# Kernel optimization log

Hardware: AMD Instinct MI355X
Metric: run time of the kernel (lower is better)

## Reference

```python
import jax, jax.numpy as jnp
import numpy as np

EPS = 1e-5
K = 20


def knn_idx(x, k):
    # x: (B, C, N) -> idx: (B, N, k) of nearest neighbors (self included)
    sq = jnp.sum(x * x, axis=1)  # (B, N)
    # pd[b,n,m] = -||x_n - x_m||^2
    pd = 2.0 * jnp.einsum('bcn,bcm->bnm', x, x) - sq[:, :, None] - sq[:, None, :]
    return jax.lax.top_k(pd, k)[1]


def graph_feature(x, k):
    # x: (B, C, N) -> (B, N, k, 2C) = concat(center, neighbor - center)
    idx = knn_idx(x, k)
    xt = jnp.transpose(x, (0, 2, 1))  # (B, N, C)
    nbr = jax.vmap(lambda t, i: t[i])(xt, idx)  # (B, N, k, C)
    ctr = jnp.broadcast_to(xt[:, :, None, :], nbr.shape)
    return jnp.concatenate([ctr, nbr - ctr], axis=-1)


def conv_bn_lrelu2d(feat, w, g, b):
    # 1x1 Conv2d (bias=False) + BatchNorm2d (training stats) + LeakyReLU(0.2)
    y = jnp.einsum('bnkc,oc->bonk', feat, w)  # (B, O, N, k)
    m = jnp.mean(y, axis=(0, 2, 3), keepdims=True)
    v = jnp.var(y, axis=(0, 2, 3), keepdims=True)
    y = (y - m) / jnp.sqrt(v + EPS) * g[None, :, None, None] + b[None, :, None, None]
    return jax.nn.leaky_relu(y, 0.2)


def reference(x, w1, g1, b1, w2, g2, b2, w3, g3, b3, w4, g4, b4, w5, g5, b5):
    x1 = jnp.max(conv_bn_lrelu2d(graph_feature(x, K), w1, g1, b1), axis=-1)   # (B, 64, N)
    x2 = jnp.max(conv_bn_lrelu2d(graph_feature(x1, K), w2, g2, b2), axis=-1)  # (B, 64, N)
    x3 = jnp.max(conv_bn_lrelu2d(graph_feature(x2, K), w3, g3, b3), axis=-1)  # (B, 128, N)
    x4 = jnp.max(conv_bn_lrelu2d(graph_feature(x3, K), w4, g4, b4), axis=-1)  # (B, 256, N)
    xc = jnp.concatenate([x1, x2, x3, x4], axis=1)  # (B, 512, N)
    y = jnp.einsum('bcn,oc->bon', xc, w5)  # (B, 1024, N)
    m = jnp.mean(y, axis=(0, 2), keepdims=True)
    v = jnp.var(y, axis=(0, 2), keepdims=True)
    y = (y - m) / jnp.sqrt(v + EPS) * g5[None, :, None] + b5[None, :, None]
    y = jax.nn.leaky_relu(y, 0.2)
    return jnp.max(y, axis=-1)  # (B, 1024)


def setup_inputs() -> dict:
    key = jax.random.key(0)
    ks = jax.random.split(key, 6)
    B, N = 8, 2048
    s = 0.02
    return {
        'x': jax.random.normal(ks[0], (B, 3, N), dtype=jnp.float32),
        'w1': jax.random.normal(ks[1], (64, 6), dtype=jnp.float32) * s,
        'g1': jnp.ones((64,), jnp.float32), 'b1': jnp.zeros((64,), jnp.float32),
        'w2': jax.random.normal(ks[2], (64, 128), dtype=jnp.float32) * s,
        'g2': jnp.ones((64,), jnp.float32), 'b2': jnp.zeros((64,), jnp.float32),
        'w3': jax.random.normal(ks[3], (128, 128), dtype=jnp.float32) * s,
        'g3': jnp.ones((128,), jnp.float32), 'b3': jnp.zeros((128,), jnp.float32),
        'w4': jax.random.normal(ks[4], (256, 256), dtype=jnp.float32) * s,
        'g4': jnp.ones((256,), jnp.float32), 'b4': jnp.zeros((256,), jnp.float32),
        'w5': jax.random.normal(ks[5], (1024, 512), dtype=jnp.float32) * s,
        'g5': jnp.ones((1024,), jnp.float32), 'b5': jnp.zeros((1024,), jnp.float32),
    }
```

## Files before the change

### kernel.cpp

```cpp
#include <hip/hip_runtime.h>
#include <hip/hip_bf16.h>
#include <math.h>

#define BB 8
#define NN 2048
#define KK 20
#define XCCH 512
#define NSLOT 64
#define LEPS 1e-5f
#define NEGINF -3.4e38f

typedef __attribute__((ext_vector_type(8))) short s8v;
typedef __attribute__((ext_vector_type(8))) _Float16 h8v;
typedef __attribute__((ext_vector_type(4))) float f32x4;

__device__ __forceinline__ float lrelu(float x){ return x >= 0.f ? x : 0.2f*x; }

__global__ __launch_bounds__(256) void k_transpose(const float* __restrict__ x, float* __restrict__ xt){
  int i = blockIdx.x*256 + threadIdx.x;
  if (i >= BB*NN) return;
  int b = i >> 11, n = i & (NN-1);
  float4 v;
  v.x = x[(b*3+0)*NN + n];
  v.y = x[(b*3+1)*NN + n];
  v.z = x[(b*3+2)*NN + n];
  v.w = 0.f;
  reinterpret_cast<float4*>(xt)[i] = v;
}

__global__ __launch_bounds__(256) void k_cvtw(const float* __restrict__ W, __hip_bfloat16* __restrict__ Wb,
                                              int Cs, int coff, int Ccnt, int Cpad, int total){
  int i = blockIdx.x*256 + threadIdx.x;
  if (i >= total) return;
  int o = i / Cpad, c = i - o*Cpad;
  Wb[i] = (c < Ccnt) ? __float2bfloat16(W[(size_t)o*Cs + coff + c]) : __float2bfloat16(0.f);
}

__global__ __launch_bounds__(256) void k_split(const float* __restrict__ P, int stride, int Ci, int Cpad,
    _Float16* __restrict__ Ph, _Float16* __restrict__ Pl){
  int i = blockIdx.x*256 + threadIdx.x;
  if (i >= BB*NN*Cpad) return;
  int p = i / Cpad, c = i - p*Cpad;
  float v = (c < Ci) ? P[(size_t)p*stride + c] : 0.f;
  _Float16 h = (_Float16)v;
  float r = v - (float)h;
  Ph[i] = h;
  Pl[i] = (_Float16)r;
}

__global__ __launch_bounds__(256) void k_sqs(const _Float16* __restrict__ Ph,
    const _Float16* __restrict__ Pl, int Cpad, float* __restrict__ sq){
  int i = blockIdx.x*256 + threadIdx.x;
  if (i >= BB*NN) return;
  const _Float16* ph = Ph + (size_t)i*Cpad;
  const _Float16* pl = Pl + (size_t)i*Cpad;
  float s = 0.f;
  for (int c = 0; c < Cpad; ++c){
    float v = (float)ph[c] + (float)pl[c];
    s += v*v;
  }
  sq[i] = s;
}

__global__ __launch_bounds__(256) void k_distm(
    const _Float16* __restrict__ Ph, const _Float16* __restrict__ Pl,
    int Cpad, int nchunk, const float* __restrict__ sq, float* __restrict__ pd)
{
  __shared__ _Float16 Ah[128*40];
  __shared__ _Float16 Al[128*40];
  __shared__ _Float16 Bh[128*40];
  __shared__ _Float16 Bl[128*40];
  int t = threadIdx.x;
  int w = t >> 6, lane = t & 63, m = lane & 15, quad = lane >> 4;
  int b = blockIdx.z;
  int i = blockIdx.x;
  int by = (int)((sqrtf(8.f*(float)i + 1.f) - 1.f) * 0.5f);
  while ((by+1)*(by+2)/2 <= i) by++;
  while (by*(by+1)/2 > i) by--;
  int bx = i - by*(by+1)/2;
  int n0 = by * 128, m0 = bx * 128;
  const _Float16* PhB = Ph + (size_t)b*NN*Cpad;
  const _Float16* PlB = Pl + (size_t)b*NN*Cpad;
  f32x4 acc[2][8];
  #pragma unroll
  for (int s=0;s<2;s++)
    #pragma unroll
    for (int j=0;j<8;j++){ f32x4 z = {0.f,0.f,0.f,0.f}; acc[s][j] = z; }
  int r = t >> 1;
  int sg0 = t & 1;
  for (int ch=0; ch<nchunk; ++ch){
    int c0 = ch*32;
    #pragma unroll
    for (int k=0;k<2;k++){
      int seg = sg0 + 2*k;
      int go = c0 + seg*8;
      size_t an = (size_t)(n0+r)*Cpad + go;
      size_t bm = (size_t)(m0+r)*Cpad + go;
      *(h8v*)&Ah[r*40 + seg*8] = *(const h8v*)&PhB[an];
      *(h8v*)&Al[r*40 + seg*8] = *(const h8v*)&PlB[an];
      *(h8v*)&Bh[r*40 + seg*8] = *(const h8v*)&PhB[bm];
      *(h8v*)&Bl[r*40 + seg*8] = *(const h8v*)&PlB[bm];
    }
    __syncthreads();
    h8v ah0 = *(const h8v*)&Ah[(w*32 + m)*40 + quad*8];
    h8v al0 = *(const h8v*)&Al[(w*32 + m)*40 + quad*8];
    h8v ah1 = *(const h8v*)&Ah[(w*32 + 16 + m)*40 + quad*8];
    h8v al1 = *(const h8v*)&Al[(w*32 + 16 + m)*40 + quad*8];
    #pragma unroll
    for (int j=0;j<8;j++){
      h8v bh = *(const h8v*)&Bh[(j*16 + m)*40 + quad*8];
      h8v bl = *(const h8v*)&Bl[(j*16 + m)*40 + quad*8];
      acc[0][j] = __builtin_amdgcn_mfma_f32_16x16x32_f16(ah0, bh, acc[0][j], 0, 0, 0);
      acc[0][j] = __builtin_amdgcn_mfma_f32_16x16x32_f16(ah0, bl, acc[0][j], 0, 0, 0);
      acc[0][j] = __builtin_amdgcn_mfma_f32_16x16x32_f16(al0, bh, acc[0][j], 0, 0, 0);
      acc[0][j] = __builtin_amdgcn_mfma_f32_16x16x32_f16(al0, bl, acc[0][j], 0, 0, 0);
      acc[1][j] = __builtin_amdgcn_mfma_f32_16x16x32_f16(ah1, bh, acc[1][j], 0, 0, 0);
      acc[1][j] = __builtin_amdgcn_mfma_f32_16x16x32_f16(ah1, bl, acc[1][j], 0, 0, 0);
      acc[1][j] = __builtin_amdgcn_mfma_f32_16x16x32_f16(al1, bh, acc[1][j], 0, 0, 0);
      acc[1][j] = __builtin_amdgcn_mfma_f32_16x16x32_f16(al1, bl, acc[1][j], 0, 0, 0);
    }
    __syncthreads();
  }
  float sqm_[8];
  #pragma unroll
  for (int j=0;j<8;j++) sqm_[j] = sq[b*NN + m0 + j*16 + m];
  float sqn_[2][4];
  #pragma unroll
  for (int s=0;s<2;s++)
    #pragma unroll
    for (int rg=0; rg<4; rg++)
      sqn_[s][rg] = sq[b*NN + n0 + w*32 + s*16 + quad*4 + rg];
  #pragma unroll
  for (int s=0;s<2;s++){
    #pragma unroll
    for (int rg=0; rg<4; rg++){
      size_t rowoff = ((size_t)b*NN + n0 + w*32 + s*16 + quad*4 + rg)*NN + m0 + m;
      #pragma unroll
      for (int j=0;j<8;j++){
        pd[rowoff + j*16] = 2.f*acc[s][j][rg] - sqn_[s][rg] - sqm_[j];
      }
    }
  }
  if (bx != by){
    #pragma unroll
    for (int s=0;s<2;s++){
      #pragma unroll
      for (int j=0;j<8;j++){
        size_t moff = ((size_t)b*NN + m0 + j*16 + m)*NN + n0 + w*32 + s*16 + quad*4;
        float4 v;
        v.x = 2.f*acc[s][j][0] - sqm_[j] - sqn_[s][0];
        v.y = 2.f*acc[s][j][1] - sqm_[j] - sqn_[s][1];
        v.z = 2.f*acc[s][j][2] - sqm_[j] - sqn_[s][2];
        v.w = 2.f*acc[s][j][3] - sqm_[j] - sqn_[s][3];
        *(float4*)&pd[moff] = v;
      }
    }
  }
}

#define TK_REP32(F) F(0)F(1)F(2)F(3)F(4)F(5)F(6)F(7)F(8)F(9)F(10)F(11)F(12)F(13)F(14)F(15) \
                    F(16)F(17)F(18)F(19)F(20)F(21)F(22)F(23)F(24)F(25)F(26)F(27)F(28)F(29)F(30)F(31)
#define TK3_SCAN(u) { bool c1 = r##u > p1; bool c2 = r##u > p2; bool c3 = r##u > p3; \
    p3 = c2 ? p2 : (c3 ? r##u : p3); \
    i2 = c1 ? i1 : (c2 ? u : i2); \
    p2 = c1 ? p1 : (c2 ? r##u : p2); \
    i1 = c1 ? u : i1; \
    p1 = c1 ? r##u : p1; }
#define TK3_RSCAN(u) { float vv = ((rem >> u) & 1u) ? NEGINF : r##u; \
    bool c1 = vv > p1; bool c2 = vv > p2; bool c3 = vv > p3; \
    p3 = c2 ? p2 : (c3 ? vv : p3); \
    i2 = c1 ? i1 : (c2 ? u : i2); \
    p2 = c1 ? p1 : (c2 ? vv : p2); \
    i1 = c1 ? u : i1; \
    p1 = c1 ? vv : p1; }

__global__ __launch_bounds__(256) void k_topk(const float* __restrict__ pd, int* __restrict__ idxo){
  int t = threadIdx.x;
  int l = t & 63;
  int row = blockIdx.x*4 + (t >> 6);
  const float4* rp = (const float4*)(pd + (size_t)row*NN);
  float4 q0 = rp[0*64+l], q1 = rp[1*64+l], q2 = rp[2*64+l], q3 = rp[3*64+l];
  float4 q4 = rp[4*64+l], q5 = rp[5*64+l], q6 = rp[6*64+l], q7 = rp[7*64+l];
  float r0 =q0.x, r1 =q0.y, r2 =q0.z, r3 =q0.w, r4 =q1.x, r5 =q1.y, r6 =q1.z, r7 =q1.w;
  float r8 =q2.x, r9 =q2.y, r10=q2.z, r11=q2.w, r12=q3.x, r13=q3.y, r14=q3.z, r15=q3.w;
  float r16=q4.x, r17=q4.y, r18=q4.z, r19=q4.w, r20=q5.x, r21=q5.y, r22=q5.z, r23=q5.w;
  float r24=q6.x, r25=q6.y, r26=q6.z, r27=q6.w, r28=q7.x, r29=q7.y, r30=q7.z, r31=q7.w;
  float p1 = NEGINF, p2 = NEGINF, p3 = NEGINF;
  int i1 = 0, i2 = 0, nv = 3;
  unsigned rem = 0u;
  TK_REP32(TK3_SCAN)
  int* orow = idxo + (size_t)row*KK;
  int got = 0;
  while (got < KK){
    float M2 = p2;
    #pragma unroll
    for (int off=1; off<64; off<<=1) M2 = fmaxf(M2, __shfl_xor(M2, off));
    bool ex = (p1 >= M2);
    unsigned long long ball = __ballot(ex);
    int cnt = __popcll(ball);
    int take = KK - got;
    if (cnt <= take){
      if (ex){
        int pos = got + __popcll(ball & ((1ull << l) - 1ull));
        orow[pos] = ((i1 >> 2) << 8) | (l << 2) | (i1 & 3);
        rem |= 1u << i1;
        p1 = p2; i1 = i2; p2 = p3; nv--;
      }
      got += cnt;
      if (got < KK && nv < 2){
        p1 = NEGINF; p2 = NEGINF; p3 = NEGINF; i1 = 0; i2 = 0;
        TK_REP32(TK3_RSCAN)
        nv = 3;
      }
    } else {
      for (int tt = 0; tt < take; ++tt){
        float wv = p1;
        #pragma unroll
        for (int off=1; off<64; off<<=1) wv = fmaxf(wv, __shfl_xor(wv, off));
        int gi = (p1 == wv) ? (((i1 >> 2) << 8) | (l << 2) | (i1 & 3)) : 0x7FFFFFFF;
        int cand = gi;
        #pragma unroll
        for (int off=1; off<64; off<<=1){
          int oc = __shfl_xor(cand, off);
          cand = oc < cand ? oc : cand;
        }
        if (gi == cand){
          orow[got + tt] = cand;
          p1 = NEGINF;
        }
      }
      got = KK;
    }
  }
}

__global__ __launch_bounds__(256) void k_wprep(const float* __restrict__ W, int Ci, int Oi,
                                               float* __restrict__ W2){
  int i = blockIdx.x*256 + threadIdx.x;
  if (i >= 2*Oi*Ci) return;
  int r = i / Ci, c = i - r*Ci;
  if (r < Oi){
    W2[i] = W[(size_t)r*2*Ci + Ci + c];
  } else {
    int o = r - Oi;
    W2[i] = W[(size_t)o*2*Ci + c] - W[(size_t)o*2*Ci + Ci + c];
  }
}

__global__ __launch_bounds__(256) void k_gemmud(const float* __restrict__ P, int stride, int Ci,
    const float* __restrict__ W2, int ostr, float* __restrict__ udb){
  __shared__ float Pt[16*68];
  __shared__ float Wt[16*68];
  int t = threadIdx.x, ty = t >> 4, tx = t & 15;
  int p0 = blockIdx.x*64, o0 = blockIdx.y*64;
  float acc[4][4];
  #pragma unroll
  for (int i=0;i<4;i++)
    #pragma unroll
    for (int j=0;j<4;j++) acc[i][j]=0.f;
  for (int c0 = 0; c0 < Ci; c0 += 16){
    #pragma unroll
    for (int q=0;q<4;q++){
      int e = t + 256*q;
      int r = e >> 4, cc = e & 15;
      int c = c0 + cc;
      bool ok = (c < Ci);
      Pt[cc*68 + r] = ok ? P[(size_t)(p0+r)*stride + c] : 0.f;
      Wt[cc*68 + r] = ok ? W2[(size_t)(o0+r)*Ci + c] : 0.f;
    }
    __syncthreads();
    #pragma unroll
    for (int j=0;j<16;j++){
      float4 av  = *(const float4*)&Pt[j*68 + ty*4];
      float4 bv4 = *(const float4*)&Wt[j*68 + tx*4];
      float a[4]  = {av.x, av.y, av.z, av.w};
      float bv[4] = {bv4.x, bv4.y, bv4.z, bv4.w};
      #pragma unroll
      for (int i=0;i<4;i++)
        #pragma unroll
        for (int jj=0;jj<4;jj++) acc[i][jj] += a[i]*bv[jj];
    }
    __syncthreads();
  }
  #pragma unroll
  for (int i=0;i<4;i++){
    *(float4*)&udb[(size_t)(p0+ty*4+i)*ostr + o0 + tx*4] =
      make_float4(acc[i][0], acc[i][1], acc[i][2], acc[i][3]);
  }
}

__global__ __launch_bounds__(256) void k_edge(const float* __restrict__ udb, int ostr, int Oi,
    const int* __restrict__ idxg,
    float* __restrict__ ymax, float* __restrict__ ymin,
    float* __restrict__ chsum, float* __restrict__ chsq){
  __shared__ int lidx[16*KK];
  __shared__ float reds[2][4][64];
  int t = threadIdx.x, w = t >> 6, lane = t & 63;
  int n0 = blockIdx.x*16;
  int b  = n0 >> 11;
  int o0 = blockIdx.y*64;
  for (int q=t; q<16*KK; q+=256) lidx[q] = idxg[(size_t)n0*KK + q];
  __syncthreads();
  int o = o0 + lane;
  float ws_s = 0.f, ws_q = 0.f;
  #pragma unroll
  for (int p=0;p<4;p++){
    int pl = w*4 + p;
    int n = n0 + pl;
    float mx = -3.4e38f, mn = 3.4e38f, s = 0.f, s2 = 0.f;
    #pragma unroll
    for (int k=0;k<KK;k++){
      int nb = lidx[pl*KK + k];
      float u = udb[(size_t)((b<<11) + nb)*ostr + o];
      mx = fmaxf(mx, u); mn = fminf(mn, u);
      s += u; s2 += u*u;
    }
    float Dv = udb[(size_t)n*ostr + Oi + o];
    size_t base = (size_t)n*256 + o;
    ymax[base] = mx + Dv;
    ymin[base] = mn + Dv;
    ws_s += s + (float)KK*Dv;
    ws_q += s2 + 2.f*Dv*s + (float)KK*Dv*Dv;
  }
  reds[0][w][lane] = ws_s;
  reds[1][w][lane] = ws_q;
  __syncthreads();
  if (w == 0){
    float s = reds[0][0][lane] + reds[0][1][lane] + reds[0][2][lane] + reds[0][3][lane];
    float q = reds[1][0][lane] + reds[1][1][lane] + reds[1][2][lane] + reds[1][3][lane];
    int slot = blockIdx.x & (NSLOT-1);
    atomicAdd(&chsum[slot*256 + o], s);
    atomicAdd(&chsq [slot*256 + o], q);
  }
}

__global__ __launch_bounds__(256) void k_bnstats(const float* __restrict__ chsum, const float* __restrict__ chsq,
    const float* __restrict__ g, const float* __restrict__ bet,
    float* __restrict__ scl, float* __restrict__ shf, int Oi){
  int o = threadIdx.x;
  if (o >= Oi) return;
  float s=0.f, s2=0.f;
  for (int u=0;u<NSLOT;u++){ s += chsum[u*256+o]; s2 += chsq[u*256+o]; }
  float cnt = (float)(BB*NN*KK);
  float mean = s/cnt;
  float var = s2/cnt - mean*mean;
  float sc = g[o] / sqrtf(var + LEPS);
  scl[o] = sc;
  shf[o] = bet[o] - mean*sc;
}

__global__ __launch_bounds__(256) void k_apply(const float* __restrict__ ymax, const float* __restrict__ ymin,
    const float* __restrict__ scl, const float* __restrict__ shf,
    float* __restrict__ xc, __hip_bfloat16* __restrict__ xcb, int off, int Oi){
  int i = blockIdx.x*256 + threadIdx.x;
  if (i >= BB*NN*Oi) return;
  int o = i & (Oi-1);
  size_t p = (size_t)((unsigned)i / (unsigned)Oi);
  float sc = scl[o];
  float v = (sc >= 0.f) ? ymax[p*256+o] : ymin[p*256+o];
  float r = lrelu(v*sc + shf[o]);
  xc [p*XCCH + off + o] = r;
  xcb[p*XCCH + off + o] = __float2bfloat16(r);
}

__global__ __launch_bounds__(256) void k_conv5m(const __hip_bfloat16* __restrict__ xcb,
    const __hip_bfloat16* __restrict__ w5b,
    float* __restrict__ pmax, float* __restrict__ pmin,
    float* __restrict__ psum, float* __restrict__ psq)
{
  __shared__ __align__(16) char smem[20480];
  __hip_bfloat16* As = (__hip_bfloat16*)smem;
  __hip_bfloat16* Bs = (__hip_bfloat16*)(smem + 10240);
  float* red = (float*)smem;
  int t = threadIdx.x, w = t >> 6, lane = t & 63, m = lane & 15, quad = lane >> 4;
  int nbk = blockIdx.x;
  int b = blockIdx.z;
  int o0 = blockIdx.y * 128;
  int n0 = nbk * 128;
  const __hip_bfloat16* Abase = xcb + (size_t)(b*NN + n0)*XCCH;
  const __hip_bfloat16* Bbase = w5b + (size_t)o0*XCCH;
  f32x4 acc[2][8];
  #pragma unroll
  for (int s=0;s<2;s++)
    #pragma unroll
    for (int j=0;j<8;j++){ f32x4 z = {0.f,0.f,0.f,0.f}; acc[s][j] = z; }
  int r = t >> 1;
  int sg0 = t & 1;
  for (int ch=0; ch<16; ++ch){
    int c0 = ch*32;
    #pragma unroll
    for (int k=0;k<2;k++){
      int seg = sg0 + 2*k;
      int go = c0 + seg*8;
      *(s8v*)&As[r*40 + seg*8] = *(const s8v*)&Abase[(size_t)r*XCCH + go];
      *(s8v*)&Bs[r*40 + seg*8] = *(const s8v*)&Bbase[(size_t)r*XCCH + go];
    }
    __syncthreads();
    s8v a0 = *(const s8v*)&As[(w*32 + m)*40 + quad*8];
    s8v a1 = *(const s8v*)&As[(w*32 + 16 + m)*40 + quad*8];
    #pragma unroll
    for (int j=0;j<8;j++){
      s8v bf = *(const s8v*)&Bs[(j*16 + m)*40 + quad*8];
      acc[0][j] = __builtin_amdgcn_mfma_f32_16x16x32_bf16(a0, bf, acc[0][j], 0, 0, 0);
      acc[1][j] = __builtin_amdgcn_mfma_f32_16x16x32_bf16(a1, bf, acc[1][j], 0, 0, 0);
    }
    __syncthreads();
  }
  float mx[8], mn[8], sm[8], sq[8];
  #pragma unroll
  for (int j=0;j<8;j++){
    mx[j] = -3.4e38f; mn[j] = 3.4e38f; sm[j] = 0.f; sq[j] = 0.f;
    #pragma unroll
    for (int s=0;s<2;s++){
      f32x4 a = acc[s][j];
      #pragma unroll
      for (int rg=0; rg<4; rg++){
        float v = a[rg];
        mx[j] = fmaxf(mx[j], v); mn[j] = fminf(mn[j], v);
        sm[j] += v; sq[j] += v*v;
      }
    }
  }
  #pragma unroll
  for (int j=0;j<8;j++){
    #pragma unroll
    for (int off=16; off<=32; off<<=1){
      mx[j] = fmaxf(mx[j], __shfl_xor(mx[j], off));
      mn[j] = fminf(mn[j], __shfl_xor(mn[j], off));
      sm[j] += __shfl_xor(sm[j], off);
      sq[j] += __shfl_xor(sq[j], off);
    }
  }
  if (quad == 0){
    #pragma unroll
    for (int j=0;j<8;j++){
      int c = j*16 + m;
      red[(0*4 + w)*128 + c] = mx[j];
      red[(1*4 + w)*128 + c] = mn[j];
      red[(2*4 + w)*128 + c] = sm[j];
      red[(3*4 + w)*128 + c] = sq[j];
    }
  }
  __syncthreads();
  if (t < 128){
    int c = t;
    float MX = red[(0*4+0)*128+c], MN = red[(1*4+0)*128+c];
    float S  = red[(2*4+0)*128+c], Q  = red[(3*4+0)*128+c];
    #pragma unroll
    for (int u=1;u<4;u++){
      MX = fmaxf(MX, red[(0*4+u)*128+c]);
      MN = fminf(MN, red[(1*4+u)*128+c]);
      S += red[(2*4+u)*128+c];
      Q += red[(3*4+u)*128+c];
    }
    size_t ii = ((size_t)b*1024 + o0 + c)*16 + nbk;
    pmax[ii] = MX; pmin[ii] = MN; psum[ii] = S; psq[ii] = Q;
  }
}

__global__ __launch_bounds__(256) void k_stats5(const float* __restrict__ psum, const float* __restrict__ psq,
    const float* __restrict__ g5, const float* __restrict__ b5,
    float* __restrict__ sc5, float* __restrict__ sh5){
  int o = blockIdx.x*256 + threadIdx.x;
  float s=0.f, s2=0.f;
  for (int b=0;b<BB;b++){
    const float* ps = &psum[((size_t)b*1024 + o)*16];
    const float* pq = &psq [((size_t)b*1024 + o)*16];
    #pragma unroll
    for (int u=0;u<16;u++){ s += ps[u]; s2 += pq[u]; }
  }
  float cnt = (float)(BB*NN);
  float mean = s/cnt;
  float var = s2/cnt - mean*mean;
  float sc = g5[o] / sqrtf(var + LEPS);
  sc5[o] = sc;
  sh5[o] = b5[o] - mean*sc;
}

__global__ __launch_bounds__(256) void k_apply5(const float* __restrict__ pmax, const float* __restrict__ pmin,
    const float* __restrict__ sc5, const float* __restrict__ sh5, float* __restrict__ out){
  int i = blockIdx.x*256 + threadIdx.x;
  int o = i & 1023;
  float sc = sc5[o];
  float v;
  if (sc >= 0.f){
    const float* p = &pmax[(size_t)i*16];
    v = p[0];
    #pragma unroll
    for (int u=1;u<16;u++) v = fmaxf(v, p[u]);
  } else {
    const float* p = &pmin[(size_t)i*16];
    v = p[0];
    #pragma unroll
    for (int u=1;u<16;u++) v = fminf(v, p[u]);
  }
  out[i] = lrelu(v*sc + sh5[o]);
}

extern "C" void kernel_launch(void* const* d_in, const int* in_sizes, int n_in,
                              void* d_out, int out_size, void* d_ws, size_t ws_size,
                              hipStream_t stream){
  const float* x  = (const float*)d_in[0];
  const float* w1 = (const float*)d_in[1];
  const float* g1 = (const float*)d_in[2];
  const float* b1 = (const float*)d_in[3];
  const float* w2 = (const float*)d_in[4];
  const float* g2 = (const float*)d_in[5];
  const float* b2 = (const float*)d_in[6];
  const float* w3 = (const float*)d_in[7];
  const float* g3 = (const float*)d_in[8];
  const float* b3 = (const float*)d_in[9];
  const float* w4 = (const float*)d_in[10];
  const float* g4 = (const float*)d_in[11];
  const float* b4 = (const float*)d_in[12];
  const float* w5 = (const float*)d_in[13];
  const float* g5 = (const float*)d_in[14];
  const float* b5 = (const float*)d_in[15];
  float* out = (float*)d_out;
  float* ws = (float*)d_ws;

  const size_t F_PD   = 0;
  const size_t F_XT0  = F_PD   + (size_t)BB*NN*NN;
  const size_t F_XC   = F_XT0  + (size_t)BB*NN*4;
  const size_t F_CHS  = F_XC   + (size_t)BB*NN*XCCH;
  const size_t F_CHQ  = F_CHS  + (size_t)NSLOT*256;
  const size_t F_SCL  = F_CHQ  + (size_t)NSLOT*256;
  const size_t F_SHF  = F_SCL  + 256;
  const size_t F_SQ   = F_SHF  + 256;
  const size_t F_IDX  = F_SQ   + (size_t)BB*NN;
  const size_t F_PMAX = F_IDX  + (size_t)BB*NN*KK;
  const size_t F_PMIN = F_PMAX + (size_t)BB*1024*8;
  const size_t F_PSUM = F_PMIN + (size_t)BB*1024*8;
  const size_t F_PSQ  = F_PSUM + (size_t)BB*1024*8;
  const size_t F_SC5  = F_PSQ  + (size_t)BB*1024*8;
  const size_t F_SH5  = F_SC5  + 1024;
  const size_t F_XCB  = F_SH5  + 1024;
  const size_t F_WB   = F_XCB  + (size_t)BB*NN*XCCH/2;
  const size_t F_PH   = F_WB   + 278528;
  const size_t F_PL   = F_PH   + 1048576;

  float* pd    = ws + F_PD;
  float* udb   = pd;
  float* w2buf = pd + (size_t)12*1024*1024;
  float* ymax  = pd + (size_t)16*1024*1024;
  float* ymin  = pd + (size_t)21*1024*1024;
  float* pmax  = pd;
  float* pmin  = pd + (size_t)(1<<20);
  float* psum  = pd + (size_t)(2<<20);
  float* psq   = pd + (size_t)(3<<20);
  float* xt0   = ws + F_XT0;
  float* xc    = ws + F_XC;
  float* chsum = ws + F_CHS;
  float* chsq  = ws + F_CHQ;
  float* scl   = ws + F_SCL;
  float* shf   = ws + F_SHF;
  float* sqb   = ws + F_SQ;
  int*   idxb  = (int*)(ws + F_IDX);
  float* sc5   = ws + F_SC5;
  float* sh5   = ws + F_SH5;
  __hip_bfloat16* xcb = (__hip_bfloat16*)(ws + F_XCB);
  __hip_bfloat16* wb  = (__hip_bfloat16*)(ws + F_WB);
  __hip_bfloat16* w5b = wb + 32768;
  _Float16* Ph  = (_Float16*)(ws + F_PH);
  _Float16* Pl  = (_Float16*)(ws + F_PL);

  (void)in_sizes; (void)n_in; (void)out_size; (void)ws_size;

  k_transpose<<<64, 256, 0, stream>>>(x, xt0);
  k_cvtw<<<(524288+255)/256, 256, 0, stream>>>(w5, w5b, 512, 0, 512, 512, 524288);

  struct LayerP { const float* P; int stride; int Ci; int CiD; int Cpad;
                  const float* W; const float* g; const float* b; int Oi; int off; };
  LayerP L[4] = {
    { xt0,    4,   3,   4,   32,  w1, g1, b1,  64, 0   },
    { xc,     512, 64,  64,  64,  w2, g2, b2,  64, 64  },
    { xc+64,  512, 64,  64,  64,  w3, g3, b3, 128, 128 },
    { xc+128, 512, 128, 128, 128, w4, g4, b4, 256, 256 },
  };

  for (int l=0; l<4; ++l){
    int Cpad = L[l].Cpad, nchunk = Cpad/32;
    int Oi = L[l].Oi, Ci = L[l].Ci;
    int ostr = 2*Oi;
    k_split<<<(BB*NN*Cpad+255)/256, 256, 0, stream>>>(L[l].P, L[l].stride, L[l].CiD, Cpad, Ph, Pl);
    k_sqs<<<64, 256, 0, stream>>>(Ph, Pl, Cpad, sqb);
    k_distm<<<dim3(136,1,8), 256, 0, stream>>>(Ph, Pl, Cpad, nchunk, sqb, pd);
    k_topk<<<BB*NN/4, 256, 0, stream>>>(pd, idxb);
    hipMemsetAsync(chsum, 0, (size_t)NSLOT*256*2*sizeof(float), stream);
    k_wprep<<<(2*Oi*Ci+255)/256, 256, 0, stream>>>(L[l].W, Ci, Oi, w2buf);
    k_gemmud<<<dim3(BB*NN/64, ostr/64), 256, 0, stream>>>(L[l].P, L[l].stride, Ci, w2buf, ostr, udb);
    k_edge<<<dim3(BB*NN/16, Oi/64), 256, 0, stream>>>(udb, ostr, Oi, idxb, ymax, ymin, chsum, chsq);
    k_bnstats<<<1, 256, 0, stream>>>(chsum, chsq, L[l].g, L[l].b, scl, shf, Oi);
    k_apply<<<(BB*NN*Oi + 255)/256, 256, 0, stream>>>(ymax, ymin, scl, shf, xc, xcb, L[l].off, Oi);
  }

  k_conv5m<<<dim3(16, 8, BB), 256, 0, stream>>>(xcb, w5b, pmax, pmin, psum, psq);
  k_stats5<<<4, 256, 0, stream>>>(psum, psq, g5, b5, sc5, sh5);
  k_apply5<<<(BB*1024)/256, 256, 0, stream>>>(pmax, pmin, sc5, sh5, out);
}
```

Before: 676.4 us.

## Use split-fp16 MFMA GEMM for layer 4 and fuse fp16 split into apply

Layer 4's pointwise GEMM (Ci=128, 512 outputs) moves from a scalar fp32 FMA kernel to an MFMA kernel that uses hi/lo fp16 splits of activations and weights, with four products per tile to keep near-fp32 accuracy. The apply kernel now also writes the hi/lo fp16 split of its output for the next layer, which removes the separate split kernel for layers 2-4. It also skips the fp32 xc write for layers whose outputs are only read through the fp16 split. The cost is four MFMAs per tile plus extra fp16 stores in apply, and the result depends on the split-fp16 precision holding.

After: 646.4 us. -4.4%, faster.

```diff
diff --git a/kernel.cpp b/kernel.cpp
--- a/kernel.cpp
+++ b/kernel.cpp
@@ -289,6 +289,88 @@
   }
 }
 
+__global__ __launch_bounds__(256) void k_wprep2(const float* __restrict__ W, int Ci, int Cpad, int Oi,
+                                                _Float16* __restrict__ W2h, _Float16* __restrict__ W2l){
+  int i = blockIdx.x*256 + threadIdx.x;
+  if (i >= 2*Oi*Cpad) return;
+  int rr = i / Cpad, c = i - rr*Cpad;
+  float v = 0.f;
+  if (c < Ci){
+    if (rr < Oi) v = W[(size_t)rr*2*Ci + Ci + c];
+    else { int o = rr - Oi; v = W[(size_t)o*2*Ci + c] - W[(size_t)o*2*Ci + Ci + c]; }
+  }
+  _Float16 h = (_Float16)v;
+  W2h[i] = h;
+  W2l[i] = (_Float16)(v - (float)h);
+}
+
+__global__ __launch_bounds__(256) void k_gemmudm(
+    const _Float16* __restrict__ Ph, const _Float16* __restrict__ Pl,
+    int Cpad, int nchunk,
+    const _Float16* __restrict__ W2h, const _Float16* __restrict__ W2l,
+    int ostr, float* __restrict__ udb)
+{
+  __shared__ _Float16 Ah[128*40];
+  __shared__ _Float16 Al[128*40];
+  __shared__ _Float16 Bh[128*40];
+  __shared__ _Float16 Bl[128*40];
+  int t = threadIdx.x;
+  int w = t >> 6, lane = t & 63, m = lane & 15, quad = lane >> 4;
+  int p0 = blockIdx.x * 128, o0 = blockIdx.y * 128;
+  f32x4 acc[2][8];
+  #pragma unroll
+  for (int s=0;s<2;s++)
+    #pragma unroll
+    for (int j=0;j<8;j++){ f32x4 z = {0.f,0.f,0.f,0.f}; acc[s][j] = z; }
+  int r = t >> 1;
+  int sg0 = t & 1;
+  for (int ch=0; ch<nchunk; ++ch){
+    int c0 = ch*32;
+    #pragma unroll
+    for (int k=0;k<2;k++){
+      int seg = sg0 + 2*k;
+      int go = c0 + seg*8;
+      size_t an = (size_t)(p0+r)*Cpad + go;
+      size_t bm = (size_t)(o0+r)*Cpad + go;
+      *(h8v*)&Ah[r*40 + seg*8] = *(const h8v*)&Ph[an];
+      *(h8v*)&Al[r*40 + seg*8] = *(const h8v*)&Pl[an];
+      *(h8v*)&Bh[r*40 + seg*8] = *(const h8v*)&W2h[bm];
+      *(h8v*)&Bl[r*40 + seg*8] = *(const h8v*)&W2l[bm];
+    }
+    __syncthreads();
+    h8v ah0 = *(const h8v*)&Ah[(w*32 + m)*40 + quad*8];
+    h8v al0 = *(const h8v*)&Al[(w*32 + m)*40 + quad*8];
+    h8v ah1 = *(const h8v*)&Ah[(w*32 + 16 + m)*40 + quad*8];
+    h8v al1 = *(const h8v*)&Al[(w*32 + 16 + m)*40 + quad*8];
+    #pragma unroll
+    for (int j=0;j<8;j++){
+      h8v bh = *(const h8v*)&Bh[(j*16 + m)*40 + quad*8];
+      h8v bl = *(const h8v*)&Bl[(j*16 + m)*40 + quad*8];
+      acc[0][j] = __builtin_amdgcn_mfma_f32_16x16x32_f16(ah0, bh, acc[0][j], 0, 0, 0);
+      acc[0][j] = __builtin_amdgcn_mfma_f32_16x16x32_f16(ah0, bl, acc[0][j], 0, 0, 0);
+      acc[0][j] = __builtin_amdgcn_mfma_f32_16x16x32_f16(al0, bh, acc[0][j], 0, 0, 0);
+      acc[0][j] = __builtin_amdgcn_mfma_f32_16x16x32_f16(al0, bl, acc[0][j], 0, 0, 0);
+      acc[1][j] = __builtin_amdgcn_mfma_f32_16x16x32_f16(ah1, bh, acc[1][j], 0, 0, 0);
+      acc[1][j] = __builtin_amdgcn_mfma_f32_16x16x32_f16(ah1, bl, acc[1][j], 0, 0, 0);
+      acc[1][j] = __builtin_amdgcn_mfma_f32_16x16x32_f16(al1, bh, acc[1][j], 0, 0, 0);
+      acc[1][j] = __builtin_amdgcn_mfma_f32_16x16x32_f16(al1, bl, acc[1][j], 0, 0, 0);
+    }
+    __syncthreads();
+  }
+  #pragma unroll
+  for (int s=0;s<2;s++){
+    int rbase = w*32 + s*16 + quad*4;
+    #pragma unroll
+    for (int rg=0; rg<4; rg++){
+      size_t rowoff = (size_t)(p0 + rbase + rg)*ostr + o0 + m;
+      #pragma unroll
+      for (int j=0;j<8;j++){
+        udb[rowoff + j*16] = acc[s][j][rg];
+      }
+    }
+  }
+}
+
 __global__ __launch_bounds__(256) void k_edge(const float* __restrict__ udb, int ostr, int Oi,
     const int* __restrict__ idxg,
     float* __restrict__ ymax, float* __restrict__ ymin,
@@ -351,7 +433,8 @@
 
 __global__ __launch_bounds__(256) void k_apply(const float* __restrict__ ymax, const float* __restrict__ ymin,
     const float* __restrict__ scl, const float* __restrict__ shf,
-    float* __restrict__ xc, __hip_bfloat16* __restrict__ xcb, int off, int Oi){
+    float* __restrict__ xc, __hip_bfloat16* __restrict__ xcb, int off, int Oi,
+    _Float16* __restrict__ Phn, _Float16* __restrict__ Pln, int Cnext, int writeXc){
   int i = blockIdx.x*256 + threadIdx.x;
   if (i >= BB*NN*Oi) return;
   int o = i & (Oi-1);
@@ -359,8 +442,13 @@
   float sc = scl[o];
   float v = (sc >= 0.f) ? ymax[p*256+o] : ymin[p*256+o];
   float r = lrelu(v*sc + shf[o]);
-  xc [p*XCCH + off + o] = r;
+  if (writeXc) xc[p*XCCH + off + o] = r;
   xcb[p*XCCH + off + o] = __float2bfloat16(r);
+  if (Cnext){
+    _Float16 h = (_Float16)r;
+    Phn[p*Cnext + o] = h;
+    Pln[p*Cnext + o] = (_Float16)(r - (float)h);
+  }
 }
 
 __global__ __launch_bounds__(256) void k_conv5m(const __hip_bfloat16* __restrict__ xcb,
@@ -542,6 +630,8 @@
   float* pd    = ws + F_PD;
   float* udb   = pd;
   float* w2buf = pd + (size_t)12*1024*1024;
+  _Float16* W2h = (_Float16*)(pd + (size_t)12*1024*1024 + 65536);
+  _Float16* W2l = W2h + 65536;
   float* ymax  = pd + (size_t)16*1024*1024;
   float* ymin  = pd + (size_t)21*1024*1024;
   float* pmax  = pd;
@@ -577,21 +667,30 @@
     { xc+64,  512, 64,  64,  64,  w3, g3, b3, 128, 128 },
     { xc+128, 512, 128, 128, 128, w4, g4, b4, 256, 256 },
   };
+  int CnextA[4]  = { 64, 64, 128, 0 };
+  int writeXcA[4] = { 1, 1, 0, 0 };
 
   for (int l=0; l<4; ++l){
     int Cpad = L[l].Cpad, nchunk = Cpad/32;
     int Oi = L[l].Oi, Ci = L[l].Ci;
     int ostr = 2*Oi;
-    k_split<<<(BB*NN*Cpad+255)/256, 256, 0, stream>>>(L[l].P, L[l].stride, L[l].CiD, Cpad, Ph, Pl);
+    if (l == 0)
+      k_split<<<(BB*NN*Cpad+255)/256, 256, 0, stream>>>(L[l].P, L[l].stride, L[l].CiD, Cpad, Ph, Pl);
     k_sqs<<<64, 256, 0, stream>>>(Ph, Pl, Cpad, sqb);
     k_distm<<<dim3(136,1,8), 256, 0, stream>>>(Ph, Pl, Cpad, nchunk, sqb, pd);
     k_topk<<<BB*NN/4, 256, 0, stream>>>(pd, idxb);
     hipMemsetAsync(chsum, 0, (size_t)NSLOT*256*2*sizeof(float), stream);
-    k_wprep<<<(2*Oi*Ci+255)/256, 256, 0, stream>>>(L[l].W, Ci, Oi, w2buf);
-    k_gemmud<<<dim3(BB*NN/64, ostr/64), 256, 0, stream>>>(L[l].P, L[l].stride, Ci, w2buf, ostr, udb);
+    if (l < 3){
+      k_wprep<<<(2*Oi*Ci+255)/256, 256, 0, stream>>>(L[l].W, Ci, Oi, w2buf);
+      k_gemmud<<<dim3(BB*NN/64, ostr/64), 256, 0, stream>>>(L[l].P, L[l].stride, Ci, w2buf, ostr, udb);
+    } else {
+      k_wprep2<<<(2*Oi*Cpad+255)/256, 256, 0, stream>>>(L[l].W, Ci, Cpad, Oi, W2h, W2l);
+      k_gemmudm<<<dim3(BB*NN/128, ostr/128), 256, 0, stream>>>(Ph, Pl, Cpad, nchunk, W2h, W2l, ostr, udb);
+    }
     k_edge<<<dim3(BB*NN/16, Oi/64), 256, 0, stream>>>(udb, ostr, Oi, idxb, ymax, ymin, chsum, chsq);
     k_bnstats<<<1, 256, 0, stream>>>(chsum, chsq, L[l].g, L[l].b, scl, shf, Oi);
-    k_apply<<<(BB*NN*Oi + 255)/256, 256, 0, stream>>>(ymax, ymin, scl, shf, xc, xcb, L[l].off, Oi);
+    k_apply<<<(BB*NN*Oi + 255)/256, 256, 0, stream>>>(ymax, ymin, scl, shf, xc, xcb, L[l].off, Oi,
+                                                      Ph, Pl, CnextA[l], writeXcA[l]);
   }
 
   k_conv5m<<<dim3(16, 8, BB), 256, 0, stream>>>(xcb, w5b, pmax, pmin, psum, psq);
```
